# Kernel tuning notes

Hardware: AMD Instinct MI355X
Metric: run time of the kernel (lower is better)

Reference implementation:

```python
import jax, jax.numpy as jnp
import numpy as np

B, S = 512, 256
NUM_LOC, NUM_USERS, D = 50000, 10000, 256
MAX_RECENT = 5
DQ = D // 4            # user/hour/weekday embed dim
TEMP = 3 * DQ          # temporal feature size
H2 = D // 2            # scorer hidden
NEG = -1e9


def setup_inputs() -> dict:
    key = jax.random.key(0)
    ks = jax.random.split(key, 25)
    p = lambda i, shape: jax.random.normal(ks[i], shape, jnp.float32) * 0.02

    locations = jax.random.randint(ks[0], (B, S), 0, NUM_LOC)
    users = jax.random.randint(ks[1], (B, S), 0, NUM_USERS)
    weekdays = jax.random.randint(ks[2], (B, S), 0, 8)
    start_mins = jax.random.randint(ks[3], (B, S), 0, 1440)
    lengths = jax.random.randint(ks[4], (B,), 1, S + 1)  # ragged valid lengths
    mask = jnp.arange(S)[None, :] < lengths[:, None]     # (B,S) bool prefix mask

    return {
        "locations": locations, "users": users, "weekdays": weekdays,
        "start_mins": start_mins, "mask": mask,
        # embedding tables (padding_idx=0 row zeroed, matching torch init)
        "loc_table": p(5, (NUM_LOC, D)).at[0].set(0.0),
        "user_table": p(6, (NUM_USERS, DQ)).at[0].set(0.0),
        "hour_table": p(7, (25, DQ)).at[0].set(0.0),
        "wd_table": p(8, (8, DQ)).at[0].set(0.0),
        # LSTM (PyTorch layout: gates i,f,g,o stacked)
        "W_ih": p(9, (4 * D, D + TEMP)), "W_hh": p(10, (4 * D, D)),
        "b_ih": p(11, (4 * D,)), "b_hh": p(12, (4 * D,)),
        # recent-location scorer MLP
        "sc_W1": p(13, (H2, D + 2)), "sc_b1": p(14, (H2,)),
        "sc_W2": p(15, (1, H2)), "sc_b2": p(16, (1,)),
        # new-location predictor MLP (dropout is identity in eval)
        "np_W1": p(17, (D, D)), "np_b1": p(18, (D,)),
        "np_W2": p(19, (NUM_LOC, D)), "np_b2": p(20, (NUM_LOC,)),
        # mix predictor
        "mx_W": p(21, (1, D)), "mx_b": p(22, (1,)),
    }


def _forward(locations, users, weekdays, start_mins, mask,
             loc_table, user_table, hour_table, wd_table,
             W_ih, W_hh, b_ih, b_hh,
             sc_W1, sc_b1, sc_W2, sc_b2,
             np_W1, np_b1, np_W2, np_b2, mx_W, mx_b):
    gelu = lambda x: jax.nn.gelu(x, approximate=False)  # torch nn.GELU default

    hours = jnp.clip(start_mins // 60, 0, 24)
    temporal = jnp.concatenate(
        [user_table[users], hour_table[hours], wd_table[weekdays]], axis=-1)
    x = jnp.concatenate([loc_table[locations], temporal], axis=-1)  # (B,S,D+TEMP)

    # --- LSTM over time via scan (PyTorch gate order i,f,g,o) ---
    def step(carry, xt):
        h, c = carry
        g = xt @ W_ih.T + b_ih + h @ W_hh.T + b_hh
        i, f, gg, o = jnp.split(g, 4, axis=-1)
        c = jax.nn.sigmoid(f) * c + jax.nn.sigmoid(i) * jnp.tanh(gg)
        h = jax.nn.sigmoid(o) * jnp.tanh(c)
        return (h, c), h

    h0 = jnp.zeros((x.shape[0], D), x.dtype)
    _, outs = jax.lax.scan(step, (h0, h0), jnp.swapaxes(x, 0, 1))
    output = jnp.swapaxes(outs, 0, 1)  # (B,S,D)

    seq_lens = mask.sum(axis=1).astype(jnp.int32) - 1  # last valid index
    bids = jnp.arange(output.shape[0])
    context = output[bids, seq_lens]                   # (B,D)

    # --- vectorized ragged recent-location scoring (j=0 is last visit) ---
    j = jnp.arange(MAX_RECENT)
    idx = seq_lens[:, None] - j[None, :]               # (B,R) indices from end
    valid = idx >= 0                                   # j < seq_len_b
    idxc = jnp.clip(idx, 0, S - 1)
    bidx = bids[:, None]
    rlocs = locations[bidx, idxc]                      # (B,R)
    rtimes = start_mins[bidx, idxc]
    cur_time = start_mins[bids, seq_lens][:, None]
    tdiff = ((cur_time - rtimes).astype(jnp.float32) / 1440.0)[..., None]
    pos = jnp.broadcast_to(j.astype(jnp.float32), rlocs.shape)[..., None]
    feats = jnp.concatenate([loc_table[rlocs], tdiff, pos], axis=-1)  # (B,R,D+2)
    scores = (gelu(feats @ sc_W1.T + sc_b1) @ sc_W2.T + sc_b2)[..., 0]  # (B,R)

    # drop entry jj if some newer valid entry j' < jj has the same location.
    eq = rlocs[:, :, None] == rlocs[:, None, :]        # (B, jj, j')
    newer = (j[:, None] > j[None, :])[None]            # jj > j'
    dup = jnp.any(eq & newer & valid[:, None, :], axis=-1)
    keep = valid & ~dup
    scatter_locs = jnp.where(keep, rlocs, NUM_LOC)     # out-of-range -> dropped

    recent_logits = jnp.full((rlocs.shape[0], NUM_LOC), NEG, jnp.float32)
    recent_logits = recent_logits.at[bidx, scatter_locs].set(scores, mode='drop')

    new_logits = gelu(context @ np_W1.T + np_b1) @ np_W2.T + np_b2  # (B,NUM_LOC)
    mix = jax.nn.sigmoid(context @ mx_W.T + mx_b) * 0.9 + 0.05     # (B,1)
    return mix * recent_logits + (1.0 - mix) * new_logits


def reference(locations, users, weekdays, start_mins, mask,
              loc_table, user_table, hour_table, wd_table,
              W_ih, W_hh, b_ih, b_hh,
              sc_W1, sc_b1, sc_W2, sc_b2,
              np_W1, np_b1, np_W2, np_b2, mx_W, mx_b):
    return _forward(locations, users, weekdays, start_mins, mask,
                    loc_table, user_table, hour_table, wd_table,
                    W_ih, W_hh, b_ih, b_hh,
                    sc_W1, sc_b1, sc_W2, sc_b2,
                    np_W1, np_b1, np_W2, np_b2, mx_W, mx_b)
```

## Files before the change

kernel.cpp:

```cpp
#include <hip/hip_runtime.h>
#include <hip/hip_bf16.h>
#include <math.h>

#define B_ 512
#define S_ 256
#define D_ 256
#define NLOC 50000
#define KX 448
#define G4 1024
#define NEGV -1000000000.0f

typedef __attribute__((ext_vector_type(8))) short short8;
typedef __attribute__((ext_vector_type(4))) float f32x4;

__device__ __forceinline__ float sigmoidf_(float x){ return 1.0f/(1.0f+expf(-x)); }
__device__ __forceinline__ float geluf_(float x){ return 0.5f*x*(1.0f+erff(x*0.70710678118654752f)); }
__device__ __forceinline__ unsigned short f2bf_(float x){
  __hip_bfloat16 h = __float2bfloat16(x);
  return *(unsigned short*)&h;
}
__device__ __forceinline__ float bf2f_(unsigned short u){
  __hip_bfloat16 h = *(__hip_bfloat16*)&u;
  return __bfloat162float(h);
}
__device__ __forceinline__ float fsig_(float x){
  return __fdividef(1.0f, 1.0f + __expf(-x));
}
__device__ __forceinline__ float ftanh2_(float x){
  float ax = fabsf(x);
  float x2 = x*x;
  float tp = x*(1.0f + x2*(-0.3333333333f + x2*(0.1333333333f + x2*(-0.05396825397f))));
  float e  = __expf(2.0f*fminf(ax, 15.0f));
  float te = 1.0f - __fdividef(2.0f, e + 1.0f);
  te = copysignf(te, x);
  return ax < 0.25f ? tp : te;
}
__device__ __forceinline__ void gld_lds16_(const void* gsrc, void* ldst){
  __builtin_amdgcn_global_load_lds((const __attribute__((address_space(1))) void*)gsrc,
                                   (__attribute__((address_space(3))) void*)ldst, 16, 0, 0);
}

__global__ void k_init(int* flag){
  if (blockIdx.x==0 && threadIdx.x==0) *flag = 0;
}

__global__ void k_detect(const unsigned char* m, int* flag){
  int i = blockIdx.x*256 + threadIdx.x;
  if ((i & 1) && i < B_*S_ && m[i]) atomicOr(flag, 1);
}

__global__ void k_seqlen(const void* mp, const int* flag, int* slens){
  int b = blockIdx.x*256 + threadIdx.x;
  if (b >= B_) return;
  int cnt = 0;
  if (*flag){
    const unsigned char* m = (const unsigned char*)mp;
    for (int s=0;s<S_;s++) cnt += (m[b*S_+s] != 0);
  } else {
    const int* m = (const int*)mp;
    for (int s=0;s<S_;s++) cnt += (m[b*S_+s] != 0);
  }
  slens[b] = cnt - 1;
}

__global__ void k_buildw(const float* wih, const float* bih, const float* bhh,
                         unsigned short* Wihbf, float* btot){
  int i = blockIdx.x*256 + threadIdx.x;
  if (i < G4*KX) Wihbf[i] = f2bf_(wih[i]);
  if (i < G4) btot[i] = bih[i] + bhh[i];
}

__global__ void k_packw(const float* __restrict__ whh, unsigned char* __restrict__ Ww8){
  int idx = blockIdx.x*256 + threadIdx.x;
  if (idx >= 32768) return;
  int lane = idx & 63, f = (idx>>6)&7, kt = (idx>>9)&7, w = idx>>12;
  int q = f>>1, nt = f&1, l16 = lane&15, quad = lane>>4;
  int row = q*256 + w*32 + nt*16 + l16;
  int col = kt*32 + quad*8;
  const float* s = whh + (size_t)row*256 + col;
  unsigned lo, hi;
  lo = __builtin_amdgcn_cvt_pk_fp8_f32(s[0], s[1], 0, 0);
  lo = __builtin_amdgcn_cvt_pk_fp8_f32(s[2], s[3], lo, 1);
  hi = __builtin_amdgcn_cvt_pk_fp8_f32(s[4], s[5], 0, 0);
  hi = __builtin_amdgcn_cvt_pk_fp8_f32(s[6], s[7], hi, 1);
  uint2 v; v.x = lo; v.y = hi;
  *(uint2*)(Ww8 + (size_t)idx*8) = v;
}

__global__ __launch_bounds__(256) void k_gx(
    const int* __restrict__ loc, const int* __restrict__ usr,
    const int* __restrict__ wdy, const int* __restrict__ sm,
    const float* __restrict__ loct, const float* __restrict__ usert,
    const float* __restrict__ hourt, const float* __restrict__ wdt,
    const unsigned short* __restrict__ Wihbf, const float* __restrict__ btot,
    unsigned short* __restrict__ Gx){
  __shared__ unsigned short As[128][40];
  int tid = threadIdx.x;
  int n0 = blockIdx.x*128, m0 = blockIdx.y*128;
  int w = tid>>6, lane = tid&63;
  int quad = lane>>4, l16 = lane&15;
  int mw = (w>>1)*64, nw = (w&1)*64;
  f32x4 acc[4][4] = {};
  int r0 = tid>>2, seg = tid&3;
  for (int kt=0; kt<14; kt++){
    int k0 = kt*32;
    int kc = k0 + seg*8;
    #pragma unroll
    for (int rr=0; rr<2; rr++){
      int r = r0 + rr*64;
      int row = m0 + r;
      const float* src;
      if (kc < 256)      src = loct  + (size_t)loc[row]*256 + kc;
      else if (kc < 320) src = usert + (size_t)usr[row]*64 + (kc-256);
      else if (kc < 384) { int s = sm[row]; int hh = s/60; if (hh>24) hh=24; if (hh<0) hh=0;
                           src = hourt + (size_t)hh*64 + (kc-320); }
      else               src = wdt   + (size_t)wdy[row]*64 + (kc-384);
      float4 v0 = *(const float4*)(src);
      float4 v1 = *(const float4*)(src+4);
      short8 pk;
      pk[0]=f2bf_(v0.x); pk[1]=f2bf_(v0.y); pk[2]=f2bf_(v0.z); pk[3]=f2bf_(v0.w);
      pk[4]=f2bf_(v1.x); pk[5]=f2bf_(v1.y); pk[6]=f2bf_(v1.z); pk[7]=f2bf_(v1.w);
      *(short8*)&As[r][seg*8] = pk;
    }
    __syncthreads();
    short8 bfrag[4], afrag[4];
    #pragma unroll
    for (int nt=0; nt<4; nt++)
      bfrag[nt] = *(const short8*)(Wihbf + (size_t)(n0+nw+nt*16+l16)*KX + k0 + quad*8);
    #pragma unroll
    for (int mt=0; mt<4; mt++)
      afrag[mt] = *(const short8*)&As[mw+mt*16+l16][quad*8];
    #pragma unroll
    for (int mt=0; mt<4; mt++)
      #pragma unroll
      for (int nt=0; nt<4; nt++)
        acc[mt][nt] = __builtin_amdgcn_mfma_f32_16x16x32_bf16(afrag[mt], bfrag[nt], acc[mt][nt], 0, 0, 0);
    __syncthreads();
  }
  #pragma unroll
  for (int nt=0; nt<4; nt++){
    int col = n0 + nw + nt*16 + l16;
    float bv = btot[col];
    #pragma unroll
    for (int mt=0; mt<4; mt++){
      #pragma unroll
      for (int i=0; i<4; i++){
        int row = m0 + mw + mt*16 + quad*4 + i;
        int bb = row >> 8, tt = row & 255;
        Gx[((size_t)tt*B_ + bb)*G4 + col] = f2bf_(acc[mt][nt][i] + bv);
      }
    }
  }
}

#define CONSUME8(BATCH, CBASE) \
  _Pragma("unroll") \
  for (int j=0;j<8;j++){ int c = (CBASE)+j; \
    acc[(c&7)>>1][c&1] = __builtin_amdgcn_mfma_f32_16x16x32_fp8_fp8( \
        af[c>>3], BATCH[j], acc[(c&7)>>1][c&1], 0, 0, 0); }

__global__ __launch_bounds__(512, 2) void k_lstm(
    const unsigned short* __restrict__ Gx,
    const unsigned char* __restrict__ Ww8,
    float* __restrict__ ctx, const int* __restrict__ slens){
  __shared__ unsigned char h_s[16*256];
  __shared__ unsigned short gx_s[16*1024];
  __shared__ unsigned char whhs[8*12288];
  int tid = threadIdx.x;
  int w = tid >> 6, lane = tid & 63;
  int quad = lane >> 4, l16 = lane & 15;
  int b0 = blockIdx.x * 16;
  int dw = w * 32;

  for (int i = tid; i < 16*256; i += 512) h_s[i] = 0;

  #pragma unroll
  for (int j=0;j<12;j++)
    gld_lds16_(Ww8 + (size_t)w*32768 + j*1024 + lane*16, &whhs[w*12288 + j*1024]);

  float cst[2][4] = {{0.f,0.f,0.f,0.f},{0.f,0.f,0.f,0.f}};
  int slq[4];
  #pragma unroll
  for (int i=0;i<4;i++) slq[i] = slens[b0 + quad*4 + i];

  asm volatile("s_waitcnt vmcnt(0) lgkmcnt(0)" ::: "memory");
  __syncthreads();

  for (int t=0; t<S_; t++){
    unsigned long long pb = (unsigned long long)Ww8;
    asm volatile("" : "+s"(pb));
    const unsigned char* sb = (const unsigned char*)pb + (size_t)w*32768 + lane*8;

    long long B1[8], B2[8], B3[8], B4[8], B5[8];
    #pragma unroll
    for (int j=0;j<8;j++) B1[j] = *(const long long*)(sb + (size_t)(24+j)*512);
    #pragma unroll
    for (int j=0;j<8;j++) B2[j] = *(const long long*)(sb + (size_t)(32+j)*512);
    __builtin_amdgcn_sched_barrier(0);

    long long af[8];
    #pragma unroll
    for (int kt=0;kt<8;kt++)
      af[kt] = *(const long long*)&h_s[l16*256 + ((((kt<<2)|quad) ^ (l16&7))<<3)];
    f32x4 acc[4][2] = {};
    #pragma unroll
    for (int c=0;c<24;c++){
      long long bfr = *(const long long*)&whhs[w*12288 + c*512 + lane*8];
      acc[(c&7)>>1][c&1] = __builtin_amdgcn_mfma_f32_16x16x32_fp8_fp8(
          af[c>>3], bfr, acc[(c&7)>>1][c&1], 0, 0, 0);
    }
    __builtin_amdgcn_sched_barrier(0);

    #pragma unroll
    for (int j=0;j<8;j++) B3[j] = *(const long long*)(sb + (size_t)(40+j)*512);
    {
      const unsigned short* src = Gx + ((size_t)t*B_ + b0)*G4 + w*2048 + lane*8;
      #pragma unroll
      for (int j=0;j<4;j++) gld_lds16_(src + j*512, &gx_s[w*2048 + j*512]);
    }
    __builtin_amdgcn_sched_barrier(0);

    CONSUME8(B1, 24)
    #pragma unroll
    for (int j=0;j<8;j++) B4[j] = *(const long long*)(sb + (size_t)(48+j)*512);
    __builtin_amdgcn_sched_barrier(0);

    CONSUME8(B2, 32)
    #pragma unroll
    for (int j=0;j<8;j++) B5[j] = *(const long long*)(sb + (size_t)(56+j)*512);
    __builtin_amdgcn_sched_barrier(0);

    CONSUME8(B3, 40)
    CONSUME8(B4, 48)
    CONSUME8(B5, 56)

    asm volatile("s_waitcnt vmcnt(0) lgkmcnt(0)" ::: "memory");
    __builtin_amdgcn_sched_barrier(0);
    __builtin_amdgcn_s_barrier();

    const unsigned int* gxw = (const unsigned int*)&gx_s[0];
    int half = l16 & 1;
    #pragma unroll
    for (int nt=0;nt<2;nt++){
      int d = dw + nt*16 + l16;
      int dbase2 = (dw + nt*16) >> 1;
      #pragma unroll
      for (int i=0;i<4;i++){
        int r = quad*4 + i;
        int base = r*512 + dbase2 + (l16>>1);
        unsigned int u0 = gxw[base];
        unsigned int u1 = gxw[base + 128];
        unsigned int u2 = gxw[base + 256];
        unsigned int u3 = gxw[base + 384];
        unsigned short s0 = half ? (unsigned short)(u0>>16) : (unsigned short)(u0&0xffff);
        unsigned short s1 = half ? (unsigned short)(u1>>16) : (unsigned short)(u1&0xffff);
        unsigned short s2 = half ? (unsigned short)(u2>>16) : (unsigned short)(u2&0xffff);
        unsigned short s3 = half ? (unsigned short)(u3>>16) : (unsigned short)(u3&0xffff);
        float gi = acc[0][nt][i] + bf2f_(s0);
        float gf = acc[1][nt][i] + bf2f_(s1);
        float gg = acc[2][nt][i] + bf2f_(s2);
        float go = acc[3][nt][i] + bf2f_(s3);
        float cn = fsig_(gf)*cst[nt][i] + fsig_(gi)*ftanh2_(gg);
        float hn = fsig_(go)*ftanh2_(cn);
        cst[nt][i] = cn;
        int p8 = __builtin_amdgcn_cvt_pk_fp8_f32(hn, hn, 0, 0);
        h_s[r*256 + (((d>>3) ^ (r&7))<<3) + (d&7)] = (unsigned char)(p8 & 0xff);
        if (t == slq[i]) ctx[(size_t)(b0 + r)*D_ + d] = hn;
      }
    }

    asm volatile("s_waitcnt lgkmcnt(0)" ::: "memory");
    __builtin_amdgcn_sched_barrier(0);
    __builtin_amdgcn_s_barrier();
  }
}

__global__ void k_post1(const float* __restrict__ ctx, const float* __restrict__ W1,
                        const float* __restrict__ b1, const float* __restrict__ mxW,
                        const float* __restrict__ mxb, float* newhid, float* mixv){
  __shared__ float cs[256];
  __shared__ float red[256];
  int b = blockIdx.x, tid = threadIdx.x;
  cs[tid] = ctx[(size_t)b*D_ + tid];
  __syncthreads();
  float a = b1[tid];
  const float* wr = W1 + (size_t)tid*D_;
  for (int k=0; k<D_; k++) a += cs[k]*wr[k];
  newhid[(size_t)b*D_ + tid] = geluf_(a);
  red[tid] = cs[tid]*mxW[tid];
  __syncthreads();
  for (int s=128; s>0; s>>=1){ if (tid<s) red[tid]+=red[tid+s]; __syncthreads(); }
  if (tid==0) mixv[b] = sigmoidf_(red[0]+mxb[0])*0.9f + 0.05f;
}

__global__ void k_recent(const int* __restrict__ loc, const int* __restrict__ sm,
                         const int* __restrict__ slens, const float* __restrict__ loct,
                         const float* __restrict__ W1, const float* __restrict__ b1,
                         const float* __restrict__ W2, const float* __restrict__ b2,
                         float* scores, int* rlocs, int* keep){
  __shared__ int rl[5], vs[5];
  __shared__ float td[5];
  __shared__ float red[128];
  int b = blockIdx.x, tid = threadIdx.x;
  int sl = slens[b];
  if (tid < 5){
    int idx = sl - tid;
    int v = idx >= 0;
    int ic = v ? idx : 0;
    rl[tid] = loc[b*S_ + ic];
    vs[tid] = v;
    int cur = sm[b*S_ + sl];
    td[tid] = (float)(cur - sm[b*S_ + ic]) * (1.0f/1440.0f);
  }
  __syncthreads();
  for (int j=0; j<5; j++){
    const float* lrow = loct + (size_t)rl[j]*D_;
    const float* wr = W1 + (size_t)tid*258;
    float a = b1[tid];
    for (int k=0; k<D_; k++) a += lrow[k]*wr[k];
    a += td[j]*wr[256] + (float)j*wr[257];
    red[tid] = geluf_(a)*W2[tid];
    __syncthreads();
    for (int s=64; s>0; s>>=1){ if (tid<s) red[tid]+=red[tid+s]; __syncthreads(); }
    if (tid==0) scores[b*5+j] = red[0] + b2[0];
    __syncthreads();
  }
  if (tid==0){
    for (int j=0; j<5; j++){
      int dup = 0;
      for (int k=0; k<j; k++) dup |= (rl[j]==rl[k]) && vs[k];
      keep[b*5+j] = vs[j] && !dup;
      rlocs[b*5+j] = rl[j];
    }
  }
}

__global__ __launch_bounds__(256) void k_final(const float* __restrict__ newhid,
    const float* __restrict__ W2, const float* __restrict__ b2,
    const float* __restrict__ mixv, float* __restrict__ out){
  __shared__ float Hs[16][260];
  __shared__ float Wl[64][65];
  int tid = threadIdx.x;
  int l0 = blockIdx.x*64, b0 = blockIdx.y*16;
  int ll = tid & 63, bq = tid >> 6;
  #pragma unroll
  for (int r=0; r<16; r++) Hs[r][tid] = newhid[(size_t)(b0+r)*D_ + tid];
  float acc[4] = {0.f,0.f,0.f,0.f};
  for (int kt=0; kt<4; kt++){
    int k0 = kt*64;
    __syncthreads();
    #pragma unroll
    for (int r=0; r<4; r++){
      int row = 4*r + bq;
      int l = l0 + row;
      Wl[row][ll] = (l < NLOC) ? W2[(size_t)l*D_ + k0 + ll] : 0.f;
    }
    __syncthreads();
    #pragma unroll
    for (int kk=0; kk<64; kk++){
      float wv = Wl[ll][kk];
      #pragma unroll
      for (int bi=0; bi<4; bi++) acc[bi] += wv * Hs[bq*4+bi][k0+kk];
    }
  }
  int l = l0 + ll;
  if (l < NLOC){
    float bias = b2[l];
    #pragma unroll
    for (int bi=0; bi<4; bi++){
      int b = b0 + bq*4 + bi;
      float mx = mixv[b];
      out[(size_t)b*NLOC + l] = mx*NEGV + (1.0f-mx)*(acc[bi] + bias);
    }
  }
}

__global__ void k_scatter(const float* __restrict__ newhid, const float* __restrict__ W2,
                          const float* __restrict__ b2, const float* __restrict__ mixv,
                          const float* __restrict__ scores, const int* __restrict__ rlocs,
                          const int* __restrict__ keep, float* out){
  int b = blockIdx.x, lane = threadIdx.x;
  float mx = mixv[b];
  for (int j=0; j<5; j++){
    if (!keep[b*5+j]) continue;
    int rl = rlocs[b*5+j];
    const float* wr = W2 + (size_t)rl*D_;
    const float* hr = newhid + (size_t)b*D_;
    float a = 0.f;
    #pragma unroll
    for (int q=0; q<4; q++){ int k = lane + 64*q; a += hr[k]*wr[k]; }
    #pragma unroll
    for (int off=32; off>0; off>>=1) a += __shfl_xor(a, off, 64);
    if (lane==0)
      out[(size_t)b*NLOC + rl] = mx*scores[b*5+j] + (1.0f-mx)*(a + b2[rl]);
  }
}

extern "C" void kernel_launch(void* const* d_in, const int* in_sizes, int n_in,
                              void* d_out, int out_size, void* d_ws, size_t ws_size,
                              hipStream_t stream){
  const int* locations   = (const int*)d_in[0];
  const int* users       = (const int*)d_in[1];
  const int* weekdays    = (const int*)d_in[2];
  const int* start_mins  = (const int*)d_in[3];
  const void* mask       = d_in[4];
  const float* loc_table = (const float*)d_in[5];
  const float* user_table= (const float*)d_in[6];
  const float* hour_table= (const float*)d_in[7];
  const float* wd_table  = (const float*)d_in[8];
  const float* W_ih      = (const float*)d_in[9];
  const float* W_hh      = (const float*)d_in[10];
  const float* b_ih      = (const float*)d_in[11];
  const float* b_hh      = (const float*)d_in[12];
  const float* sc_W1     = (const float*)d_in[13];
  const float* sc_b1     = (const float*)d_in[14];
  const float* sc_W2     = (const float*)d_in[15];
  const float* sc_b2     = (const float*)d_in[16];
  const float* np_W1     = (const float*)d_in[17];
  const float* np_b1     = (const float*)d_in[18];
  const float* np_W2     = (const float*)d_in[19];
  const float* np_b2     = (const float*)d_in[20];
  const float* mx_W      = (const float*)d_in[21];
  const float* mx_b      = (const float*)d_in[22];
  float* out = (float*)d_out;

  char* w = (char*)d_ws;
  size_t o = 0;
  auto alloc = [&](size_t bytes)->void*{ void* p = w + o; o += (bytes + 255) & ~(size_t)255; return p; };
  unsigned short* Gx    = (unsigned short*)alloc((size_t)B_*S_*G4*sizeof(short));
  unsigned short* Wihbf = (unsigned short*)alloc((size_t)G4*KX*sizeof(short));
  unsigned char*  Ww8   = (unsigned char*)alloc((size_t)G4*D_);
  float* btot   = (float*)alloc((size_t)G4*sizeof(float));
  float* ctx    = (float*)alloc((size_t)B_*D_*sizeof(float));
  float* newhid = (float*)alloc((size_t)B_*D_*sizeof(float));
  float* mixv   = (float*)alloc((size_t)B_*sizeof(float));
  float* scores = (float*)alloc((size_t)B_*5*sizeof(float));
  int*   slens  = (int*)alloc((size_t)B_*sizeof(int));
  int*   rlocs  = (int*)alloc((size_t)B_*5*sizeof(int));
  int*   keep   = (int*)alloc((size_t)B_*5*sizeof(int));
  int*   flag   = (int*)alloc(sizeof(int));

  k_init<<<1, 64, 0, stream>>>(flag);
  k_detect<<<512, 256, 0, stream>>>((const unsigned char*)mask, flag);
  k_seqlen<<<2, 256, 0, stream>>>(mask, flag, slens);
  k_buildw<<<1792, 256, 0, stream>>>(W_ih, b_ih, b_hh, Wihbf, btot);
  k_packw<<<128, 256, 0, stream>>>(W_hh, Ww8);
  k_gx<<<dim3(8,1024), 256, 0, stream>>>(locations, users, weekdays, start_mins,
                                         loc_table, user_table, hour_table, wd_table,
                                         Wihbf, btot, Gx);
  k_lstm<<<32, 512, 0, stream>>>(Gx, Ww8, ctx, slens);
  k_post1<<<512, 256, 0, stream>>>(ctx, np_W1, np_b1, mx_W, mx_b, newhid, mixv);
  k_recent<<<512, 128, 0, stream>>>(locations, start_mins, slens, loc_table,
                                    sc_W1, sc_b1, sc_W2, sc_b2, scores, rlocs, keep);
  k_final<<<dim3(782,32), 256, 0, stream>>>(newhid, np_W2, np_b2, mixv, out);
  k_scatter<<<512, 64, 0, stream>>>(newhid, np_W2, np_b2, mixv, scores, rlocs, keep, out);
}
```

Measured before the change: 2.982 ms.

## Split LSTM recurrence across 16 waves and double-buffer gate inputs

The recurrent LSTM kernel now runs 1024 threads (16 waves) per block, each wave owning 16 hidden units instead of 32. The W_hh fp8 packing is reordered to match, and each wave keeps one gate's weights in LDS while streaming the other three from global/L2. The precomputed input gate values (Gx) for the next timestep are prefetched into a second LDS buffer so their load overlaps the current step's matrix multiplies. This shortens the per-step critical path of the serial recurrence, at the cost of more waves contending for barriers and more global weight traffic per step.

```diff
diff --git a/kernel.cpp b/kernel.cpp
--- a/kernel.cpp
+++ b/kernel.cpp
@@ -73,9 +73,9 @@
 __global__ void k_packw(const float* __restrict__ whh, unsigned char* __restrict__ Ww8){
   int idx = blockIdx.x*256 + threadIdx.x;
   if (idx >= 32768) return;
-  int lane = idx & 63, f = (idx>>6)&7, kt = (idx>>9)&7, w = idx>>12;
-  int q = f>>1, nt = f&1, l16 = lane&15, quad = lane>>4;
-  int row = q*256 + w*32 + nt*16 + l16;
+  int lane = idx & 63, c = (idx>>6)&31, w = idx>>11;
+  int q = c>>3, kt = c&7, l16 = lane&15, quad = lane>>4;
+  int row = q*256 + w*16 + l16;
   int col = kt*32 + quad*8;
   const float* s = whh + (size_t)row*256 + col;
   unsigned lo, hi;
@@ -153,120 +153,125 @@
   }
 }
 
-#define CONSUME8(BATCH, CBASE) \
-  _Pragma("unroll") \
-  for (int j=0;j<8;j++){ int c = (CBASE)+j; \
-    acc[(c&7)>>1][c&1] = __builtin_amdgcn_mfma_f32_16x16x32_fp8_fp8( \
-        af[c>>3], BATCH[j], acc[(c&7)>>1][c&1], 0, 0, 0); }
-
-__global__ __launch_bounds__(512, 2) void k_lstm(
+__global__ __launch_bounds__(1024, 4) void k_lstm(
     const unsigned short* __restrict__ Gx,
     const unsigned char* __restrict__ Ww8,
     float* __restrict__ ctx, const int* __restrict__ slens){
   __shared__ unsigned char h_s[16*256];
-  __shared__ unsigned short gx_s[16*1024];
-  __shared__ unsigned char whhs[8*12288];
+  __shared__ unsigned short gx_s[2][16*1024];
+  __shared__ unsigned char whhs[16*4096];
   int tid = threadIdx.x;
   int w = tid >> 6, lane = tid & 63;
   int quad = lane >> 4, l16 = lane & 15;
   int b0 = blockIdx.x * 16;
-  int dw = w * 32;
-
-  for (int i = tid; i < 16*256; i += 512) h_s[i] = 0;
+  int dw = w * 16;
+
+  for (int i = tid; i < 16*256; i += 1024) h_s[i] = 0;
 
   #pragma unroll
-  for (int j=0;j<12;j++)
-    gld_lds16_(Ww8 + (size_t)w*32768 + j*1024 + lane*16, &whhs[w*12288 + j*1024]);
-
-  float cst[2][4] = {{0.f,0.f,0.f,0.f},{0.f,0.f,0.f,0.f}};
+  for (int j=0;j<4;j++)
+    gld_lds16_(Ww8 + (size_t)w*16384 + j*1024 + lane*16, &whhs[w*4096 + j*1024]);
+
+  float cst[4] = {0.f,0.f,0.f,0.f};
   int slq[4];
   #pragma unroll
   for (int i=0;i<4;i++) slq[i] = slens[b0 + quad*4 + i];
 
-  asm volatile("s_waitcnt vmcnt(0) lgkmcnt(0)" ::: "memory");
-  __syncthreads();
+  {
+    const unsigned short* src = Gx + (size_t)b0*G4 + w*1024 + lane*8;
+    #pragma unroll
+    for (int j=0;j<2;j++) gld_lds16_(src + j*512, &gx_s[0][w*1024 + j*512]);
+  }
+  asm volatile("s_waitcnt vmcnt(2) lgkmcnt(0)" ::: "memory");
+  __builtin_amdgcn_sched_barrier(0);
+  __builtin_amdgcn_s_barrier();
 
   for (int t=0; t<S_; t++){
+    int cur = t & 1;
     unsigned long long pb = (unsigned long long)Ww8;
     asm volatile("" : "+s"(pb));
-    const unsigned char* sb = (const unsigned char*)pb + (size_t)w*32768 + lane*8;
-
-    long long B1[8], B2[8], B3[8], B4[8], B5[8];
-    #pragma unroll
-    for (int j=0;j<8;j++) B1[j] = *(const long long*)(sb + (size_t)(24+j)*512);
-    #pragma unroll
-    for (int j=0;j<8;j++) B2[j] = *(const long long*)(sb + (size_t)(32+j)*512);
+    const unsigned char* sb = (const unsigned char*)pb + (size_t)w*16384 + lane*8;
+
+    long long G0[8], G1[8], G2[8];
+    #pragma unroll
+    for (int j=0;j<8;j++) G0[j] = *(const long long*)(sb + (size_t)(8+j)*512);
+    #pragma unroll
+    for (int j=0;j<8;j++) G1[j] = *(const long long*)(sb + (size_t)(16+j)*512);
     __builtin_amdgcn_sched_barrier(0);
 
     long long af[8];
     #pragma unroll
     for (int kt=0;kt<8;kt++)
       af[kt] = *(const long long*)&h_s[l16*256 + ((((kt<<2)|quad) ^ (l16&7))<<3)];
-    f32x4 acc[4][2] = {};
-    #pragma unroll
-    for (int c=0;c<24;c++){
-      long long bfr = *(const long long*)&whhs[w*12288 + c*512 + lane*8];
-      acc[(c&7)>>1][c&1] = __builtin_amdgcn_mfma_f32_16x16x32_fp8_fp8(
-          af[c>>3], bfr, acc[(c&7)>>1][c&1], 0, 0, 0);
-    }
-    __builtin_amdgcn_sched_barrier(0);
-
-    #pragma unroll
-    for (int j=0;j<8;j++) B3[j] = *(const long long*)(sb + (size_t)(40+j)*512);
+    f32x4 acc[4] = {};
+    #pragma unroll
+    for (int c=0;c<8;c++){
+      long long bfr = *(const long long*)&whhs[w*4096 + c*512 + lane*8];
+      acc[0] = __builtin_amdgcn_mfma_f32_16x16x32_fp8_fp8(af[c], bfr, acc[0], 0, 0, 0);
+    }
+    __builtin_amdgcn_sched_barrier(0);
+
+    asm volatile("s_waitcnt vmcnt(8)" ::: "memory");
+    __builtin_amdgcn_sched_barrier(0);
+    #pragma unroll
+    for (int j=0;j<8;j++)
+      acc[1] = __builtin_amdgcn_mfma_f32_16x16x32_fp8_fp8(af[j], G0[j], acc[1], 0, 0, 0);
+    __builtin_amdgcn_sched_barrier(0);
+
+    #pragma unroll
+    for (int j=0;j<8;j++) G2[j] = *(const long long*)(sb + (size_t)(24+j)*512);
     {
-      const unsigned short* src = Gx + ((size_t)t*B_ + b0)*G4 + w*2048 + lane*8;
+      int tn = (t < S_-1) ? t+1 : t;
+      const unsigned short* src = Gx + ((size_t)tn*B_ + b0)*G4 + w*1024 + lane*8;
       #pragma unroll
-      for (int j=0;j<4;j++) gld_lds16_(src + j*512, &gx_s[w*2048 + j*512]);
-    }
-    __builtin_amdgcn_sched_barrier(0);
-
-    CONSUME8(B1, 24)
-    #pragma unroll
-    for (int j=0;j<8;j++) B4[j] = *(const long long*)(sb + (size_t)(48+j)*512);
-    __builtin_amdgcn_sched_barrier(0);
-
-    CONSUME8(B2, 32)
-    #pragma unroll
-    for (int j=0;j<8;j++) B5[j] = *(const long long*)(sb + (size_t)(56+j)*512);
-    __builtin_amdgcn_sched_barrier(0);
-
-    CONSUME8(B3, 40)
-    CONSUME8(B4, 48)
-    CONSUME8(B5, 56)
-
-    asm volatile("s_waitcnt vmcnt(0) lgkmcnt(0)" ::: "memory");
+      for (int j=0;j<2;j++) gld_lds16_(src + j*512, &gx_s[cur^1][w*1024 + j*512]);
+    }
+    __builtin_amdgcn_sched_barrier(0);
+
+    asm volatile("s_waitcnt vmcnt(10)" ::: "memory");
+    __builtin_amdgcn_sched_barrier(0);
+    #pragma unroll
+    for (int j=0;j<8;j++)
+      acc[2] = __builtin_amdgcn_mfma_f32_16x16x32_fp8_fp8(af[j], G1[j], acc[2], 0, 0, 0);
+    __builtin_amdgcn_sched_barrier(0);
+
+    asm volatile("s_waitcnt vmcnt(2)" ::: "memory");
+    __builtin_amdgcn_sched_barrier(0);
+    #pragma unroll
+    for (int j=0;j<8;j++)
+      acc[3] = __builtin_amdgcn_mfma_f32_16x16x32_fp8_fp8(af[j], G2[j], acc[3], 0, 0, 0);
+
+    asm volatile("s_waitcnt lgkmcnt(0)" ::: "memory");
     __builtin_amdgcn_sched_barrier(0);
     __builtin_amdgcn_s_barrier();
 
-    const unsigned int* gxw = (const unsigned int*)&gx_s[0];
+    const unsigned int* gxw = (const unsigned int*)&gx_s[cur][0];
     int half = l16 & 1;
-    #pragma unroll
-    for (int nt=0;nt<2;nt++){
-      int d = dw + nt*16 + l16;
-      int dbase2 = (dw + nt*16) >> 1;
-      #pragma unroll
-      for (int i=0;i<4;i++){
-        int r = quad*4 + i;
-        int base = r*512 + dbase2 + (l16>>1);
-        unsigned int u0 = gxw[base];
-        unsigned int u1 = gxw[base + 128];
-        unsigned int u2 = gxw[base + 256];
-        unsigned int u3 = gxw[base + 384];
-        unsigned short s0 = half ? (unsigned short)(u0>>16) : (unsigned short)(u0&0xffff);
-        unsigned short s1 = half ? (unsigned short)(u1>>16) : (unsigned short)(u1&0xffff);
-        unsigned short s2 = half ? (unsigned short)(u2>>16) : (unsigned short)(u2&0xffff);
-        unsigned short s3 = half ? (unsigned short)(u3>>16) : (unsigned short)(u3&0xffff);
-        float gi = acc[0][nt][i] + bf2f_(s0);
-        float gf = acc[1][nt][i] + bf2f_(s1);
-        float gg = acc[2][nt][i] + bf2f_(s2);
-        float go = acc[3][nt][i] + bf2f_(s3);
-        float cn = fsig_(gf)*cst[nt][i] + fsig_(gi)*ftanh2_(gg);
-        float hn = fsig_(go)*ftanh2_(cn);
-        cst[nt][i] = cn;
-        int p8 = __builtin_amdgcn_cvt_pk_fp8_f32(hn, hn, 0, 0);
-        h_s[r*256 + (((d>>3) ^ (r&7))<<3) + (d&7)] = (unsigned char)(p8 & 0xff);
-        if (t == slq[i]) ctx[(size_t)(b0 + r)*D_ + d] = hn;
-      }
+    int d = dw + l16;
+    int du = w*8 + (l16>>1);
+    int chunk = d >> 3;
+    #pragma unroll
+    for (int i=0;i<4;i++){
+      int r = quad*4 + i;
+      int base = r*512 + du;
+      unsigned int u0 = gxw[base];
+      unsigned int u1 = gxw[base + 128];
+      unsigned int u2 = gxw[base + 256];
+      unsigned int u3 = gxw[base + 384];
+      unsigned short s0 = half ? (unsigned short)(u0>>16) : (unsigned short)(u0&0xffff);
+      unsigned short s1 = half ? (unsigned short)(u1>>16) : (unsigned short)(u1&0xffff);
+      unsigned short s2 = half ? (unsigned short)(u2>>16) : (unsigned short)(u2&0xffff);
+      unsigned short s3 = half ? (unsigned short)(u3>>16) : (unsigned short)(u3&0xffff);
+      float gi = acc[0][i] + bf2f_(s0);
+      float gf = acc[1][i] + bf2f_(s1);
+      float gg = acc[2][i] + bf2f_(s2);
+      float go = acc[3][i] + bf2f_(s3);
+      float cn = fsig_(gf)*cst[i] + fsig_(gi)*ftanh2_(gg);
+      float hn = fsig_(go)*ftanh2_(cn);
+      cst[i] = cn;
+      int p8 = __builtin_amdgcn_cvt_pk_fp8_f32(hn, hn, 0, 0);
+      h_s[r*256 + ((chunk ^ (r&7))<<3) + (d&7)] = (unsigned char)(p8 & 0xff);
+      if (t == slq[i]) ctx[(size_t)(b0 + r)*D_ + d] = hn;
     }
 
     asm volatile("s_waitcnt lgkmcnt(0)" ::: "memory");
@@ -448,7 +453,7 @@
   k_gx<<<dim3(8,1024), 256, 0, stream>>>(locations, users, weekdays, start_mins,
                                          loc_table, user_table, hour_table, wd_table,
                                          Wihbf, btot, Gx);
-  k_lstm<<<32, 512, 0, stream>>>(Gx, Ww8, ctx, slens);
+  k_lstm<<<32, 1024, 0, stream>>>(Gx, Ww8, ctx, slens);
   k_post1<<<512, 256, 0, stream>>>(ctx, np_W1, np_b1, mx_W, mx_b, newhid, mixv);
   k_recent<<<512, 128, 0, stream>>>(locations, start_mins, slens, loc_table,
                                     sc_W1, sc_b1, sc_W2, sc_b2, scores, rlocs, keep);
```

Result: slower. 3.070 ms (+2.9%).
